# Kernel optimization log

Hardware: AMD Instinct MI355X
Metric: run time of the kernel (lower is better)

The kernel has to match this reference:

```python
import jax, jax.numpy as jnp
import numpy as np

N, IN, OUT, H = 8192, 128, 64, 4
NEG_SLOPE = 0.2   # GATConv leaky-relu slope
EPS = 1e-5        # BatchNorm1d eps
MASK_VAL = -1e9   # masked_fill value for non-edges (finite for grad safety)


def setup_inputs() -> dict:
    key = jax.random.key(0)
    ks = jax.random.split(key, 5)
    x = jax.random.normal(ks[0], (N, IN), jnp.float32)
    adj = jax.random.randint(ks[1], (N, N), 0, 2, jnp.int32)  # dense 0/1 adjacency
    W = jax.random.normal(ks[2], (H, IN, OUT), jnp.float32) * (1.0 / np.sqrt(IN))
    a_i = jax.random.normal(ks[3], (H, OUT), jnp.float32) * (1.0 / np.sqrt(OUT))
    a_j = jax.random.normal(ks[4], (H, OUT), jnp.float32) * (1.0 / np.sqrt(OUT))
    gamma = jnp.ones((H * OUT,), jnp.float32)   # BN weight
    beta = jnp.zeros((H * OUT,), jnp.float32)   # BN bias
    return {"x": x, "adj": adj, "W": W, "a_i": a_i, "a_j": a_j,
            "gamma": gamma, "beta": beta}


def reference(x, adj, W, a_i, a_j, gamma, beta):
    # --- GATConv (dense adjacency, multi-head, concat) ---
    h = jnp.einsum('ni,hio->hno', x, W)              # [H, N, OUT]
    ei = jnp.einsum('hno,ho->hn', h, a_i)            # [H, N] source scores
    ej = jnp.einsum('hno,ho->hn', h, a_j)            # [H, N] target scores
    coe = ei[:, :, None] + ej[:, None, :]            # [H, N, N]
    coe = jnp.where(coe >= 0, coe, NEG_SLOPE * coe)  # leaky_relu
    coe = jnp.where(adj[None, :, :] == 0, MASK_VAL, coe)
    att = jax.nn.softmax(coe, axis=-1)               # segment softmax over neighbors
    out = jnp.einsum('hnm,hmo->hno', att, h)         # weighted aggregation
    out = jnp.transpose(out, (1, 0, 2)).reshape(N, H * OUT)  # concat heads
    # --- BatchNorm1d (training-mode batch stats over nodes) ---
    mean = jnp.mean(out, axis=0)
    var = jnp.var(out, axis=0)
    out = (out - mean) * jax.lax.rsqrt(var + EPS) * gamma + beta
    # --- ReLU ---
    return jax.nn.relu(out)
```

## Files before the change

kernel.cpp:

```cpp
#include <hip/hip_runtime.h>
#include <hip/hip_bf16.h>

#define NN   8192
#define IND  128
#define OUTD 64
#define NH   4
#define NEG_SLOPE 0.2f
#define BN_EPS 1e-5f

typedef __attribute__((ext_vector_type(8))) short bf16x8;
typedef __attribute__((ext_vector_type(4))) float f32x4;
typedef __attribute__((ext_vector_type(4))) int   i32x4;

static __device__ __forceinline__ short f2bf(float f) {
    union { float f; unsigned u; } v; v.f = f;
    return (short)((v.u + 0x8000u) >> 16);
}

__global__ __launch_bounds__(256) void kP_mask(const int* __restrict__ adj,
                                               unsigned int* __restrict__ bm,
                                               float* __restrict__ zreg) {
    int tid = blockIdx.x * 256 + threadIdx.x;
    for (int z = tid; z < 532608; z += 524288)
        ((f32x4*)zreg)[z] = (f32x4){0.f, 0.f, 0.f, 0.f};
    for (int wd = tid; wd < NN * NN / 32; wd += 524288) {
        const int* ap = adj + (size_t)wd * 32;
        unsigned m = 0;
#pragma unroll
        for (int q = 0; q < 8; ++q) {
            i32x4 a = *(const i32x4*)(ap + q * 4);
#pragma unroll
            for (int j = 0; j < 4; ++j)
                m |= (a[j] ? 1u : 0u) << (q * 4 + j);
        }
        bm[wd] = m;
    }
}

__global__ __launch_bounds__(256) void k0_repackW(const float* __restrict__ W,
                                                  short* __restrict__ WB) {
    int tid = blockIdx.x * 256 + threadIdx.x;
    int o = tid & 63, i = (tid >> 6) & 127, h = tid >> 13;
    WB[((h * 16 + (i >> 3)) * 64 + o) * 8 + (i & 7)] = f2bf(W[(h * 128 + i) * 64 + o]);
}

__global__ __launch_bounds__(256) void k1_feat(const float* __restrict__ x,
                                               const short* __restrict__ WB,
                                               const float* __restrict__ a_i,
                                               const float* __restrict__ a_j,
                                               short* __restrict__ hB,
                                               float* __restrict__ t_ei,  float* __restrict__ t_E1i,
                                               float* __restrict__ t_E2i, float* __restrict__ t_nj,
                                               float* __restrict__ t_E1j, float* __restrict__ t_E2j) {
    int w = threadIdx.x >> 6;
    int l = threadIdx.x & 63;
    int quad = l >> 4, lx = l & 15;
    int rb = blockIdx.x;

    f32x4 acc[4] = {};
#pragma unroll
    for (int ks = 0; ks < 4; ++ks) {
        const float* xp = x + (rb * 16 + lx) * IND + ks * 32 + quad * 8;
        f32x4 xa = *(const f32x4*)xp;
        f32x4 xb = *(const f32x4*)(xp + 4);
        bf16x8 af;
#pragma unroll
        for (int j = 0; j < 4; ++j) { af[j] = f2bf(xa[j]); af[4 + j] = f2bf(xb[j]); }
#pragma unroll
        for (int ot = 0; ot < 4; ++ot) {
            bf16x8 bf = *(const bf16x8*)(WB + ((w * 16 + ks * 4 + quad) * 64 + ot * 16 + lx) * 8);
            acc[ot] = __builtin_amdgcn_mfma_f32_16x16x32_bf16(af, bf, acc[ot], 0, 0, 0);
        }
    }
    float aiv[4], ajv[4];
#pragma unroll
    for (int ot = 0; ot < 4; ++ot) {
        aiv[ot] = a_i[w * 64 + ot * 16 + lx];
        ajv[ot] = a_j[w * 64 + ot * 16 + lx];
    }
#pragma unroll
    for (int reg = 0; reg < 4; ++reg) {
        int row = rb * 16 + quad * 4 + reg;
        float ei = 0.f, ej = 0.f;
#pragma unroll
        for (int ot = 0; ot < 4; ++ot) {
            float hv = acc[ot][reg];
            ei += hv * aiv[ot];
            ej += hv * ajv[ot];
        }
#pragma unroll
        for (int m = 1; m <= 8; m <<= 1) {
            ei += __shfl_xor(ei, m, 64);
            ej += __shfl_xor(ej, m, 64);
        }
        if (lx == reg) {
            t_ei [w * NN + row] = ei;
            t_E1i[w * NN + row] = expf(ei);
            t_E2i[w * NN + row] = expf(NEG_SLOPE * ei);
            t_nj [w * NN + row] = -ej;
            t_E1j[w * NN + row] = expf(ej);
            t_E2j[w * NN + row] = expf(NEG_SLOPE * ej);
        }
#pragma unroll
        for (int ot = 0; ot < 4; ++ot) {
            int o = ot * 16 + lx;
            hB[((w * 1024 + (row >> 3)) * 64 + o) * 8 + (row & 7)] = f2bf(acc[ot][reg]);
        }
    }
}

__global__ __launch_bounds__(256) void k2_attn(const unsigned char* __restrict__ bmb,
                                               const short* __restrict__ hB,
                                               const float* __restrict__ t_ei,
                                               const float* __restrict__ t_E1i,
                                               const float* __restrict__ t_E2i,
                                               const float* __restrict__ t_nj,
                                               const float* __restrict__ t_E1j,
                                               const float* __restrict__ t_E2j,
                                               float* __restrict__ num,
                                               float* __restrict__ Lsum) {
    int w = threadIdx.x >> 6;
    int l = threadIdx.x & 63;
    int quad = l >> 4, lx = l & 15;
    int rb = blockIdx.x >> 2, ks = blockIdx.x & 3;
    int rowbase = rb * 64;
    int tb = w * NN;

    float eiv[4], E1i[4], E2i[4];
    int mbase[4];
#pragma unroll
    for (int r = 0; r < 4; ++r) {
        int i = rowbase + r * 16 + lx;
        eiv[r] = t_ei[tb + i];
        E1i[r] = t_E1i[tb + i];
        E2i[r] = t_E2i[tb + i];
        mbase[r] = i * 1024 + ks * 256 + quad;
    }

    f32x4 acc[4][4] = {};
    float Lacc[4] = {0.f, 0.f, 0.f, 0.f};
    int k0 = ks * 2048;

    int pm[4];
    f32x4 pnj0, pnj1, pe10, pe11, pe20, pe21;
    {
        int kb = k0 + quad * 8;
        pnj0 = *(const f32x4*)(t_nj  + tb + kb);
        pnj1 = *(const f32x4*)(t_nj  + tb + kb + 4);
        pe10 = *(const f32x4*)(t_E1j + tb + kb);
        pe11 = *(const f32x4*)(t_E1j + tb + kb + 4);
        pe20 = *(const f32x4*)(t_E2j + tb + kb);
        pe21 = *(const f32x4*)(t_E2j + tb + kb + 4);
#pragma unroll
        for (int r = 0; r < 4; ++r) pm[r] = bmb[mbase[r]];
    }

#pragma unroll 1
    for (int kt = 0; kt < 64; ++kt) {
        f32x4 nj0 = pnj0, nj1 = pnj1;
        f32x4 e1j0 = pe10, e1j1 = pe11;
        f32x4 e2j0 = pe20, e2j1 = pe21;
        int mc[4];
#pragma unroll
        for (int r = 0; r < 4; ++r) mc[r] = pm[r];

        int ktn = (kt + 1) & 63;
        int kbn = k0 + ktn * 32 + quad * 8;
        pnj0 = *(const f32x4*)(t_nj  + tb + kbn);
        pnj1 = *(const f32x4*)(t_nj  + tb + kbn + 4);
        pe10 = *(const f32x4*)(t_E1j + tb + kbn);
        pe11 = *(const f32x4*)(t_E1j + tb + kbn + 4);
        pe20 = *(const f32x4*)(t_E2j + tb + kbn);
        pe21 = *(const f32x4*)(t_E2j + tb + kbn + 4);
#pragma unroll
        for (int r = 0; r < 4; ++r) pm[r] = bmb[mbase[r] + ktn * 4];

        int kb = k0 + kt * 32 + quad * 8;
        bf16x8 bfrag[4];
#pragma unroll
        for (int ot = 0; ot < 4; ++ot)
            bfrag[ot] = *(const bf16x8*)(hB + ((w * 1024 + (kb >> 3)) * 64 + ot * 16 + lx) * 8);

        bf16x8 afr[4];
#pragma unroll
        for (int r = 0; r < 4; ++r) {
            union { i32x4 i; bf16x8 b; } af;
            float lsum = 0.f;
#pragma unroll
            for (int jj = 0; jj < 4; ++jj) {
                int j0 = 2 * jj, j1 = 2 * jj + 1;
                int   av0 = mc[r] & (1 << j0);
                int   av1 = mc[r] & (1 << j1);
                float njA = (j0 < 4) ? nj0[j0] : nj1[j0 - 4];
                float njB = (j1 < 4) ? nj0[j1] : nj1[j1 - 4];
                float e1A = (j0 < 4) ? e1j0[j0] : e1j1[j0 - 4];
                float e1B = (j1 < 4) ? e1j0[j1] : e1j1[j1 - 4];
                float e2A = (j0 < 4) ? e2j0[j0] : e2j1[j0 - 4];
                float e2B = (j1 < 4) ? e2j0[j1] : e2j1[j1 - 4];
                bool  cA  = eiv[r] >= njA;
                bool  cB  = eiv[r] >= njB;
                float p0  = (cA ? E1i[r] : E2i[r]) * (cA ? e1A : e2A);
                float p1  = (cB ? E1i[r] : E2i[r]) * (cB ? e1B : e2B);
                p0 = av0 ? p0 : 0.0f;
                p1 = av1 ? p1 : 0.0f;
                lsum += p0 + p1;
                unsigned u0 = __float_as_uint(p0) + 0x8000u;
                unsigned u1 = __float_as_uint(p1) + 0x8000u;
                af.i[jj] = (int)__builtin_amdgcn_perm(u1, u0, 0x07060302);
            }
            Lacc[r] += lsum;
            afr[r] = af.b;
        }
#pragma unroll
        for (int r = 0; r < 4; ++r)
#pragma unroll
            for (int ot = 0; ot < 4; ++ot)
                acc[r][ot] = __builtin_amdgcn_mfma_f32_16x16x32_bf16(afr[r], bfrag[ot], acc[r][ot], 0, 0, 0);
    }

#pragma unroll
    for (int r = 0; r < 4; ++r) {
        float L = Lacc[r];
        L += __shfl_xor(L, 16, 64);
        L += __shfl_xor(L, 32, 64);
        if (l < 16)
            atomicAdd(&Lsum[w * NN + rowbase + r * 16 + lx], L);
    }
#pragma unroll
    for (int r = 0; r < 4; ++r)
#pragma unroll
        for (int ot = 0; ot < 4; ++ot)
#pragma unroll
            for (int reg = 0; reg < 4; ++reg) {
                int row = rowbase + r * 16 + quad * 4 + reg;
                atomicAdd(&num[row * 256 + w * 64 + ot * 16 + lx], acc[r][ot][reg]);
            }
}

__global__ __launch_bounds__(256) void k3_combine(float* __restrict__ num,
                                                  const float* __restrict__ Lsum,
                                                  float* __restrict__ stats) {
    int c = threadIdx.x;
    int h = c >> 6;
    float s = 0.f, s2 = 0.f;
    for (int rr = 0; rr < 32; ++rr) {
        int row = blockIdx.x * 32 + rr;
        float L = Lsum[h * NN + row];
        float val = num[row * 256 + c] / L;
        num[row * 256 + c] = val;
        s += val; s2 += val * val;
    }
    atomicAdd(&stats[c], s);
    atomicAdd(&stats[c + 256], s2);
}

__global__ __launch_bounds__(256) void k5_apply(const float* __restrict__ preout,
                                                const float* __restrict__ stats,
                                                const float* __restrict__ gamma,
                                                const float* __restrict__ beta,
                                                float* __restrict__ out) {
    __shared__ float sbnp[512];
    int c = threadIdx.x;
    float mean = stats[c] * (1.0f / NN);
    float var  = stats[c + 256] * (1.0f / NN) - mean * mean;
    float sc = gamma[c] * rsqrtf(var + BN_EPS);
    sbnp[c] = sc;
    sbnp[c + 256] = beta[c] - mean * sc;
    __syncthreads();

    int g = blockIdx.x * 256 + threadIdx.x;
    f32x4 v = *(const f32x4*)(preout + (size_t)g * 4);
    int cb = (g * 4) & 255;
    f32x4 r;
#pragma unroll
    for (int j = 0; j < 4; ++j)
        r[j] = fmaxf(v[j] * sbnp[cb + j] + sbnp[256 + cb + j], 0.0f);
    *(f32x4*)(out + (size_t)g * 4) = r;
}

extern "C" void kernel_launch(void* const* d_in, const int* in_sizes, int n_in,
                              void* d_out, int out_size, void* d_ws, size_t ws_size,
                              hipStream_t stream) {
    (void)in_sizes; (void)n_in; (void)out_size; (void)ws_size;
    const float* x     = (const float*)d_in[0];
    const int*   adj   = (const int*)d_in[1];
    const float* W     = (const float*)d_in[2];
    const float* a_i   = (const float*)d_in[3];
    const float* a_j   = (const float*)d_in[4];
    const float* gamma = (const float*)d_in[5];
    const float* beta  = (const float*)d_in[6];
    float* out = (float*)d_out;

    char* ws = (char*)d_ws;
    short* WB    = (short*)(ws + 0);
    short* hB    = (short*)(ws + 65536);
    float* t_ei  = (float*)(ws + 4259840);
    float* t_E1i = t_ei + 32768;
    float* t_E2i = t_ei + 2 * 32768;
    float* t_nj  = t_ei + 3 * 32768;
    float* t_E1j = t_ei + 4 * 32768;
    float* t_E2j = t_ei + 5 * 32768;
    float* num   = (float*)(ws + 5046272);
    float* Lsum  = (float*)(ws + 13434880);
    float* stats = (float*)(ws + 13565952);
    unsigned int* bm = (unsigned int*)(ws + 13568000);

    kP_mask   <<<dim3(2048), dim3(256), 0, stream>>>(adj, bm, num);
    k0_repackW<<<dim3(128),  dim3(256), 0, stream>>>(W, WB);
    k1_feat   <<<dim3(512),  dim3(256), 0, stream>>>(x, WB, a_i, a_j, hB,
                                                     t_ei, t_E1i, t_E2i, t_nj, t_E1j, t_E2j);
    k2_attn   <<<dim3(512),  dim3(256), 0, stream>>>((const unsigned char*)bm, hB,
                                                     t_ei, t_E1i, t_E2i, t_nj, t_E1j, t_E2j,
                                                     num, Lsum);
    k3_combine<<<dim3(256),  dim3(256), 0, stream>>>(num, Lsum, stats);
    k5_apply  <<<dim3(2048), dim3(256), 0, stream>>>(num, stats, gamma, beta, out);
}
```

Before: 522.1 us.

## Rescale softmax weights by exp(-ei) and compute row sums via MFMA ones

Attention weights are now rescaled by a per-row factor exp(-ei), so the positive branch is just exp(ej) and the negative branch is one multiply by a precomputed ratio exp(-0.8*ei). The per-row normaliser L is accumulated with an extra MFMA against a vector of bf16 ones instead of scalar adds and shuffles, and the bf16 conversion drops rounding for plain truncation. The row sum now uses the same bf16-quantised weights as the numerator, and k3_combine is split into more blocks with fewer rows each. Together these cut VALU work in the inner loop at the cost of four extra MFMAs per step, more atomics in k3, and slightly different rounding.

```diff
diff --git a/kernel.cpp b/kernel.cpp
--- a/kernel.cpp
+++ b/kernel.cpp
@@ -49,8 +49,8 @@
                                                const float* __restrict__ a_i,
                                                const float* __restrict__ a_j,
                                                short* __restrict__ hB,
-                                               float* __restrict__ t_ei,  float* __restrict__ t_E1i,
-                                               float* __restrict__ t_E2i, float* __restrict__ t_nj,
+                                               float* __restrict__ t_ei,  float* __restrict__ t_Ri,
+                                               float* __restrict__ t_nj,
                                                float* __restrict__ t_E1j, float* __restrict__ t_E2j) {
     int w = threadIdx.x >> 6;
     int l = threadIdx.x & 63;
@@ -95,8 +95,7 @@
         }
         if (lx == reg) {
             t_ei [w * NN + row] = ei;
-            t_E1i[w * NN + row] = expf(ei);
-            t_E2i[w * NN + row] = expf(NEG_SLOPE * ei);
+            t_Ri [w * NN + row] = expf(-0.8f * ei);
             t_nj [w * NN + row] = -ej;
             t_E1j[w * NN + row] = expf(ej);
             t_E2j[w * NN + row] = expf(NEG_SLOPE * ej);
@@ -112,8 +111,7 @@
 __global__ __launch_bounds__(256) void k2_attn(const unsigned char* __restrict__ bmb,
                                                const short* __restrict__ hB,
                                                const float* __restrict__ t_ei,
-                                               const float* __restrict__ t_E1i,
-                                               const float* __restrict__ t_E2i,
+                                               const float* __restrict__ t_Ri,
                                                const float* __restrict__ t_nj,
                                                const float* __restrict__ t_E1j,
                                                const float* __restrict__ t_E2j,
@@ -126,19 +124,22 @@
     int rowbase = rb * 64;
     int tb = w * NN;
 
-    float eiv[4], E1i[4], E2i[4];
+    float eiv[4], Riv[4];
     int mbase[4];
 #pragma unroll
     for (int r = 0; r < 4; ++r) {
         int i = rowbase + r * 16 + lx;
         eiv[r] = t_ei[tb + i];
-        E1i[r] = t_E1i[tb + i];
-        E2i[r] = t_E2i[tb + i];
+        Riv[r] = t_Ri[tb + i];
         mbase[r] = i * 1024 + ks * 256 + quad;
     }
 
+    bf16x8 onesf;
+#pragma unroll
+    for (int j = 0; j < 8; ++j) onesf[j] = (short)0x3F80;
+
     f32x4 acc[4][4] = {};
-    float Lacc[4] = {0.f, 0.f, 0.f, 0.f};
+    f32x4 accL[4] = {};
     int k0 = ks * 2048;
 
     int pm[4];
@@ -185,32 +186,28 @@
 #pragma unroll
         for (int r = 0; r < 4; ++r) {
             union { i32x4 i; bf16x8 b; } af;
-            float lsum = 0.f;
 #pragma unroll
             for (int jj = 0; jj < 4; ++jj) {
                 int j0 = 2 * jj, j1 = 2 * jj + 1;
-                int   av0 = mc[r] & (1 << j0);
-                int   av1 = mc[r] & (1 << j1);
                 float njA = (j0 < 4) ? nj0[j0] : nj1[j0 - 4];
                 float njB = (j1 < 4) ? nj0[j1] : nj1[j1 - 4];
                 float e1A = (j0 < 4) ? e1j0[j0] : e1j1[j0 - 4];
                 float e1B = (j1 < 4) ? e1j0[j1] : e1j1[j1 - 4];
                 float e2A = (j0 < 4) ? e2j0[j0] : e2j1[j0 - 4];
                 float e2B = (j1 < 4) ? e2j0[j1] : e2j1[j1 - 4];
-                bool  cA  = eiv[r] >= njA;
-                bool  cB  = eiv[r] >= njB;
-                float p0  = (cA ? E1i[r] : E2i[r]) * (cA ? e1A : e2A);
-                float p1  = (cB ? E1i[r] : E2i[r]) * (cB ? e1B : e2B);
-                p0 = av0 ? p0 : 0.0f;
-                p1 = av1 ? p1 : 0.0f;
-                lsum += p0 + p1;
-                unsigned u0 = __float_as_uint(p0) + 0x8000u;
-                unsigned u1 = __float_as_uint(p1) + 0x8000u;
-                af.i[jj] = (int)__builtin_amdgcn_perm(u1, u0, 0x07060302);
+                float p0 = (eiv[r] >= njA) ? e1A : Riv[r] * e2A;
+                float p1 = (eiv[r] >= njB) ? e1B : Riv[r] * e2B;
+                p0 = (mc[r] & (1 << j0)) ? p0 : 0.0f;
+                p1 = (mc[r] & (1 << j1)) ? p1 : 0.0f;
+                af.i[jj] = (int)__builtin_amdgcn_perm(__float_as_uint(p1),
+                                                      __float_as_uint(p0),
+                                                      0x07060302);
             }
-            Lacc[r] += lsum;
             afr[r] = af.b;
         }
+#pragma unroll
+        for (int r = 0; r < 4; ++r)
+            accL[r] = __builtin_amdgcn_mfma_f32_16x16x32_bf16(afr[r], onesf, accL[r], 0, 0, 0);
 #pragma unroll
         for (int r = 0; r < 4; ++r)
 #pragma unroll
@@ -219,13 +216,11 @@
     }
 
 #pragma unroll
-    for (int r = 0; r < 4; ++r) {
-        float L = Lacc[r];
-        L += __shfl_xor(L, 16, 64);
-        L += __shfl_xor(L, 32, 64);
-        if (l < 16)
-            atomicAdd(&Lsum[w * NN + rowbase + r * 16 + lx], L);
-    }
+    for (int r = 0; r < 4; ++r)
+        if (lx == 0)
+#pragma unroll
+            for (int reg = 0; reg < 4; ++reg)
+                atomicAdd(&Lsum[w * NN + rowbase + r * 16 + quad * 4 + reg], accL[r][reg]);
 #pragma unroll
     for (int r = 0; r < 4; ++r)
 #pragma unroll
@@ -243,8 +238,9 @@
     int c = threadIdx.x;
     int h = c >> 6;
     float s = 0.f, s2 = 0.f;
-    for (int rr = 0; rr < 32; ++rr) {
-        int row = blockIdx.x * 32 + rr;
+#pragma unroll
+    for (int rr = 0; rr < 8; ++rr) {
+        int row = blockIdx.x * 8 + rr;
         float L = Lsum[h * NN + row];
         float val = num[row * 256 + c] / L;
         num[row * 256 + c] = val;
@@ -295,11 +291,10 @@
     short* WB    = (short*)(ws + 0);
     short* hB    = (short*)(ws + 65536);
     float* t_ei  = (float*)(ws + 4259840);
-    float* t_E1i = t_ei + 32768;
-    float* t_E2i = t_ei + 2 * 32768;
-    float* t_nj  = t_ei + 3 * 32768;
-    float* t_E1j = t_ei + 4 * 32768;
-    float* t_E2j = t_ei + 5 * 32768;
+    float* t_Ri  = t_ei + 32768;
+    float* t_nj  = t_ei + 2 * 32768;
+    float* t_E1j = t_ei + 3 * 32768;
+    float* t_E2j = t_ei + 4 * 32768;
     float* num   = (float*)(ws + 5046272);
     float* Lsum  = (float*)(ws + 13434880);
     float* stats = (float*)(ws + 13565952);
@@ -308,10 +303,10 @@
     kP_mask   <<<dim3(2048), dim3(256), 0, stream>>>(adj, bm, num);
     k0_repackW<<<dim3(128),  dim3(256), 0, stream>>>(W, WB);
     k1_feat   <<<dim3(512),  dim3(256), 0, stream>>>(x, WB, a_i, a_j, hB,
-                                                     t_ei, t_E1i, t_E2i, t_nj, t_E1j, t_E2j);
+                                                     t_ei, t_Ri, t_nj, t_E1j, t_E2j);
     k2_attn   <<<dim3(512),  dim3(256), 0, stream>>>((const unsigned char*)bm, hB,
-                                                     t_ei, t_E1i, t_E2i, t_nj, t_E1j, t_E2j,
+                                                     t_ei, t_Ri, t_nj, t_E1j, t_E2j,
                                                      num, Lsum);
-    k3_combine<<<dim3(256),  dim3(256), 0, stream>>>(num, Lsum, stats);
+    k3_combine<<<dim3(1024), dim3(256), 0, stream>>>(num, Lsum, stats);
     k5_apply  <<<dim3(2048), dim3(256), 0, stream>>>(num, stats, gamma, beta, out);
 }
```

Result: slower. 534.7 us (+2.4%).
